# Kernel tuning notes

Hardware: AMD Instinct MI355X
Metric: run time of the kernel (lower is better)

Reference implementation:

```python
import jax, jax.numpy as jnp
import numpy as np

L, D, I, H, B, T, NBLK = 2, 2048, 5632, 16, 2, 1024, 4
EPS, TEMP, THETA = 1e-6, 1.0, 10000.0


def _rms_base(x):
    # RMSNorm without affine weight, computed in fp32 (matches _rms_norm_base)
    x = x.astype(jnp.float32)
    return x * jax.lax.rsqrt(jnp.mean(x * x, axis=-1, keepdims=True) + EPS)


def _rope(x):
    # x: [B,T,H,dh], rotate-half RoPE
    dh = x.shape[-1]
    inv = 1.0 / (THETA ** (jnp.arange(0, dh, 2, dtype=jnp.float32) / dh))
    t = jnp.arange(x.shape[1], dtype=jnp.float32)
    fr = jnp.outer(t, inv)  # [T, dh/2]
    cos = jnp.tile(jnp.cos(fr), (1, 2))[None, :, None, :]
    sin = jnp.tile(jnp.sin(fr), (1, 2))[None, :, None, :]
    x1, x2 = jnp.split(x, 2, axis=-1)
    return x * cos + jnp.concatenate([-x2, x1], axis=-1) * sin


def _attention(x, Wq, Wk, Wv, Wo):
    Bb, Tt, Dd = x.shape
    dh = Dd // H
    q = _rope((x @ Wq).reshape(Bb, Tt, H, dh))
    k = _rope((x @ Wk).reshape(Bb, Tt, H, dh))
    v = (x @ Wv).reshape(Bb, Tt, H, dh)
    s = jnp.einsum('bqhd,bkhd->bhqk', q, k) / jnp.sqrt(jnp.float32(dh))
    causal = jnp.tril(jnp.ones((Tt, Tt), bool))
    s = jnp.where(causal, s, jnp.float32(-1e30))
    a = jax.nn.softmax(s, axis=-1)
    return jnp.einsum('bhqk,bkhd->bqhd', a, v).reshape(Bb, Tt, Dd) @ Wo


def _forward(block_states, w_query_attn, key_norm_w_attn, w_query_mlp, key_norm_w_mlp,
             attn_norm_w, Wq, Wk, Wv, Wo, mlp_norm_w, Wgate, Wup, Wdown,
             active_mask, current_block_idx):
    n, Bb, Tt, Dd = block_states.shape
    scale = jnp.sqrt(jnp.float32(Dd)) * TEMP
    block_input = block_states[current_block_idx]
    mask = active_mask.astype(jnp.float32)[:, None, None]  # [B,1,1]

    # ---- phase 1: batch_attend_completed_blocks over all 2L routers ----
    # effective query = w_query * key_norm.weight (norm weight folded into query)
    q_eff = jnp.stack([w_query_attn * key_norm_w_attn,
                       w_query_mlp * key_norm_w_mlp], axis=1).reshape(2 * L, Dd)
    base_keys = _rms_base(block_states)                      # [n,B,T,D] fp32
    scores = jnp.einsum('qd,nbtd->qnbt', q_eff, base_keys) / scale
    mx = scores.max(axis=1)                                  # [q,B,T]
    ex = jnp.exp(scores - mx[:, None])                       # [q,n,B,T]
    lse = ex.sum(axis=1)                                     # [q,B,T]
    outs = jnp.einsum('qnbt,nbtd->qbtd', ex, block_states)   # unnormalized

    def merge(qi, partial):
        # merge_with_partial_block: online-softmax merge of phase1 stats with
        # the score of the current partial block
        if partial is None:
            return outs[qi] / lse[qi][..., None]
        ps = jnp.einsum('d,btd->bt', q_eff[qi], _rms_base(partial)) / scale
        m = jnp.maximum(mx[qi], ps)
        c1 = jnp.exp(mx[qi] - m)
        c2 = jnp.exp(ps - m)
        denom = c1 * lse[qi] + c2
        return (outs[qi] * (c1 * lse[qi] / denom)[..., None]
                + partial * (c2 / denom)[..., None])

    def blend(old, new):
        return new * mask + old * (1.0 - mask)

    def rmsn(x, w):
        return _rms_base(x) * w

    partial = None
    for i in range(L):
        attn_in = merge(2 * i, partial)
        attn_out = _attention(rmsn(attn_in, attn_norm_w[i]), Wq[i], Wk[i], Wv[i], Wo[i])
        old = block_input if partial is None else partial
        partial = blend(old, attn_out if partial is None else partial + attn_out)
        mlp_in = merge(2 * i + 1, partial)
        h = rmsn(mlp_in, mlp_norm_w[i])
        mlp_out = (jax.nn.silu(h @ Wgate[i]) * (h @ Wup[i])) @ Wdown[i]
        partial = blend(partial, partial + mlp_out)
    return partial


def setup_inputs() -> dict:
    key = jax.random.key(0)
    ks = jax.random.split(key, 12)
    p = lambda k, shape: jax.random.normal(k, shape, jnp.float32) * 0.02
    return {
        'block_states': jax.random.normal(ks[0], (NBLK, B, T, D), jnp.float32),
        'active_mask': jnp.ones((B,), bool),
        'w_query_attn': jax.random.normal(ks[1], (L, D), jnp.float32) * 0.02,
        'key_norm_w_attn': jnp.ones((L, D), jnp.float32),
        'w_query_mlp': jax.random.normal(ks[2], (L, D), jnp.float32) * 0.02,
        'key_norm_w_mlp': jnp.ones((L, D), jnp.float32),
        'attn_norm_w': jnp.ones((L, D), jnp.float32),
        'Wq': p(ks[3], (L, D, D)), 'Wk': p(ks[4], (L, D, D)),
        'Wv': p(ks[5], (L, D, D)), 'Wo': p(ks[6], (L, D, D)),
        'mlp_norm_w': jnp.ones((L, D), jnp.float32),
        'Wgate': p(ks[7], (L, D, I)), 'Wup': p(ks[8], (L, D, I)),
        'Wdown': p(ks[9], (L, I, D)),
        'current_block_idx': 3,
    }


def reference(block_states, active_mask, w_query_attn, key_norm_w_attn, w_query_mlp,
              key_norm_w_mlp, attn_norm_w, Wq, Wk, Wv, Wo, mlp_norm_w,
              Wgate, Wup, Wdown, current_block_idx):
    return _forward(block_states, w_query_attn, key_norm_w_attn, w_query_mlp,
                    key_norm_w_mlp, attn_norm_w, Wq, Wk, Wv, Wo, mlp_norm_w,
                    Wgate, Wup, Wdown, active_mask, current_block_idx)
```

## Files before the change

### kernel.cpp

```cpp
#include <hip/hip_runtime.h>

typedef unsigned short u16;
typedef __bf16 bf16x8 __attribute__((ext_vector_type(8)));
typedef float f32x4 __attribute__((ext_vector_type(4)));

__device__ __forceinline__ float u2f(unsigned int b){ union{unsigned int u; float f;} x; x.u=b; return x.f; }
__device__ __forceinline__ u16 f2b(float f){
  union{float fv; unsigned int u;} x; x.fv=f;
  unsigned int r = x.u + 0x7fffu + ((x.u>>16)&1u);
  return (u16)(r>>16);
}
__device__ __forceinline__ float b2f(u16 v){ return u2f(((unsigned int)v)<<16); }
__device__ __forceinline__ unsigned int pk2(float lo, float hi){
  return (unsigned int)f2b(lo) | ((unsigned int)f2b(hi)<<16);
}
__device__ __forceinline__ void load8(const float* p, float* o){
  float4 a = ((const float4*)p)[0], b = ((const float4*)p)[1];
  o[0]=a.x;o[1]=a.y;o[2]=a.z;o[3]=a.w;o[4]=b.x;o[5]=b.y;o[6]=b.z;o[7]=b.w;
}
__device__ __forceinline__ void gl_lds16(const u16* g, bf16x8* l){
  __builtin_amdgcn_global_load_lds((const __attribute__((address_space(1))) void*)g,
                                   (__attribute__((address_space(3))) void*)l, 16, 0, 0);
}

#define INV_SCALE 0.022097086912079608f
#define ATT_SCALE 0.08838834764831845f

__global__ __launch_bounds__(256) void mega0_kernel(
    const float* __restrict__ bs, const float* __restrict__ wqa, const float* __restrict__ kna,
    const float* __restrict__ wqm, const float* __restrict__ knm, const float* __restrict__ anw0,
    float* __restrict__ outs, float* __restrict__ mxb, float* __restrict__ lseb,
    u16* __restrict__ xnorm,
    const float* __restrict__ Wq, const float* __restrict__ Wk,
    const float* __restrict__ Wv, const float* __restrict__ Wo,
    const float* __restrict__ Wg, const float* __restrict__ Wu,
    const float* __restrict__ Wd,
    u16* __restrict__ WTall, u16* __restrict__ WTgu, u16* __restrict__ WTdd)
{
  int bb0 = blockIdx.x;
  if (bb0 < 2048){
    const int D=2048, M=2048;
    int m = bb0, t = threadIdx.x;
    int col = t*8;
    float x[4][8];
    #pragma unroll
    for (int n=0;n<4;n++) load8(bs + ((size_t)n*M + m)*D + col, x[n]);
    float qe[4][8];
    {
      float a[8], b[8];
      load8(wqa+col,a);   load8(kna+col,b);
      #pragma unroll
      for (int j=0;j<8;j++) qe[0][j]=a[j]*b[j];
      load8(wqm+col,a);   load8(knm+col,b);
      #pragma unroll
      for (int j=0;j<8;j++) qe[1][j]=a[j]*b[j];
      load8(wqa+D+col,a); load8(kna+D+col,b);
      #pragma unroll
      for (int j=0;j<8;j++) qe[2][j]=a[j]*b[j];
      load8(wqm+D+col,a); load8(knm+D+col,b);
      #pragma unroll
      for (int j=0;j<8;j++) qe[3][j]=a[j]*b[j];
    }
    float vals[20];
    #pragma unroll
    for (int n=0;n<4;n++){
      float s=0.f;
      #pragma unroll
      for (int j=0;j<8;j++) s += x[n][j]*x[n][j];
      vals[n]=s;
    }
    #pragma unroll
    for (int q=0;q<4;q++)
      #pragma unroll
      for (int n=0;n<4;n++){
        float s=0.f;
        #pragma unroll
        for (int j=0;j<8;j++) s += qe[q][j]*x[n][j];
        vals[4+q*4+n]=s;
      }
    #pragma unroll
    for (int s=0;s<20;s++){
      float v=vals[s];
      v+=__shfl_xor(v,1,64); v+=__shfl_xor(v,2,64); v+=__shfl_xor(v,4,64);
      v+=__shfl_xor(v,8,64); v+=__shfl_xor(v,16,64); v+=__shfl_xor(v,32,64);
      vals[s]=v;
    }
    __shared__ float red[20][4];
    __shared__ float redx[4];
    int w=t>>6, lane=t&63;
    if (lane==0){
      #pragma unroll
      for (int s=0;s<20;s++) red[s][w]=vals[s];
    }
    __syncthreads();
    float tot[20];
    #pragma unroll
    for (int s=0;s<20;s++) tot[s]=red[s][0]+red[s][1]+red[s][2]+red[s][3];
    float rn[4];
    #pragma unroll
    for (int n=0;n<4;n++) rn[n]=rsqrtf(tot[n]*(1.0f/2048.0f)+1e-6f);
    #pragma unroll
    for (int q=0;q<4;q++){
      float a0=tot[4+q*4+0]*rn[0]*INV_SCALE;
      float a1=tot[4+q*4+1]*rn[1]*INV_SCALE;
      float a2=tot[4+q*4+2]*rn[2]*INV_SCALE;
      float a3=tot[4+q*4+3]*rn[3]*INV_SCALE;
      float mx=fmaxf(fmaxf(a0,a1),fmaxf(a2,a3));
      float e0=__expf(a0-mx), e1=__expf(a1-mx), e2=__expf(a2-mx), e3=__expf(a3-mx);
      float lse=e0+e1+e2+e3;
      float ov[8];
      #pragma unroll
      for (int j=0;j<8;j++)
        ov[j]=e0*x[0][j]+e1*x[1][j]+e2*x[2][j]+e3*x[3][j];
      if (q==0){
        float inv = 1.0f/lse;
        float mg[8];
        #pragma unroll
        for (int j=0;j<8;j++) mg[j] = ov[j]*inv;
        float ssm=0.f;
        #pragma unroll
        for (int j=0;j<8;j++) ssm += mg[j]*mg[j];
        #pragma unroll
        for (int msk=1; msk<64; msk<<=1) ssm += __shfl_xor(ssm,msk,64);
        if (lane==0) redx[w]=ssm;
        __syncthreads();
        float st = redx[0]+redx[1]+redx[2]+redx[3];
        float r = rsqrtf(st*(1.0f/2048.0f)+1e-6f);
        float wv[8]; load8(anw0+col, wv);
        ushort4 o0, o1;
        o0.x=f2b(mg[0]*r*wv[0]); o0.y=f2b(mg[1]*r*wv[1]); o0.z=f2b(mg[2]*r*wv[2]); o0.w=f2b(mg[3]*r*wv[3]);
        o1.x=f2b(mg[4]*r*wv[4]); o1.y=f2b(mg[5]*r*wv[5]); o1.z=f2b(mg[6]*r*wv[6]); o1.w=f2b(mg[7]*r*wv[7]);
        size_t row = (size_t)m*D + col;
        ((ushort4*)(xnorm+row))[0]=o0; ((ushort4*)(xnorm+row))[1]=o1;
      } else {
        if (t==0){ mxb[(size_t)q*M+m]=mx; lseb[(size_t)q*M+m]=lse; }
        float* op = outs + ((size_t)q*M+m)*(size_t)D + col;
        float4 v0, v1;
        v0.x=ov[0]; v0.y=ov[1]; v0.z=ov[2]; v0.w=ov[3];
        v1.x=ov[4]; v1.y=ov[5]; v1.z=ov[6]; v1.w=ov[7];
        ((float4*)op)[0]=v0; ((float4*)op)[1]=v1;
      }
    }
    return;
  }
  int tid = threadIdx.x, wv = tid>>6, lane = tid&63;
  int tt = (bb0 - 2048)*4 + wv;
  const float* src; u16* dst; int K, N, kb, nb;
  if (tt < 8192){
    int z = tt >> 10, rem = tt & 1023;
    int x = rem & 31, y = rem >> 5;
    int wsel = z>>1, l = z&1;
    const float* s = (wsel==0)?Wq:(wsel==1)?Wk:(wsel==2)?Wv:Wo;
    src = s + (size_t)l*2048*2048;
    dst = WTall + (size_t)z*2048*2048;
    K=2048; N=2048; kb=y*64; nb=x*64;
  } else if (tt < 19456){
    int idx = tt - 8192;
    int z = idx / 2816, rem = idx % 2816;
    int x = rem % 88, y = rem / 88;
    int wsel = z>>1, l = z&1;
    const float* s = (wsel==0)?Wg:Wu;
    src = s + (size_t)l*2048*5632;
    dst = WTgu + (size_t)z*2048*5632;
    K=2048; N=5632; kb=y*64; nb=x*64;
  } else {
    int idx = tt - 19456;
    int l = idx / 2816, rem = idx % 2816;
    int x = rem % 32, y = rem / 32;
    src = Wd + (size_t)l*5632*2048;
    dst = WTdd + (size_t)l*5632*2048;
    K=5632; N=2048; kb=y*64; nb=x*64;
  }
  int kg = lane>>3, ng = lane&7;
  const float* sp = src + (size_t)(kb + kg*8)*N + nb + ng*8;
  float r[8][8];
  #pragma unroll
  for (int i=0;i<8;i++){
    float4 a = *(const float4*)(sp + (size_t)i*N);
    float4 b = *(const float4*)(sp + (size_t)i*N + 4);
    r[i][0]=a.x; r[i][1]=a.y; r[i][2]=a.z; r[i][3]=a.w;
    r[i][4]=b.x; r[i][5]=b.y; r[i][6]=b.z; r[i][7]=b.w;
  }
  u16* dp = dst + (size_t)(nb + ng*8)*K + kb + kg*8;
  #pragma unroll
  for (int j=0;j<8;j++){
    uint4 o;
    o.x = pk2(r[0][j], r[1][j]);
    o.y = pk2(r[2][j], r[3][j]);
    o.z = pk2(r[4][j], r[5][j]);
    o.w = pk2(r[6][j], r[7][j]);
    *(uint4*)(dp + (size_t)j*K) = o;
  }
}

__global__ __launch_bounds__(256) void ropevtrans_kernel(
    const u16* __restrict__ v, u16* __restrict__ vT,
    u16* __restrict__ qb, u16* __restrict__ kb)
{
  int bb = blockIdx.x;
  if (bb < 1024){
    __shared__ u16 tile[64][69];
    int x = bb & 15, y = (bb>>4) & 1, z = bb>>5;
    int b = z>>4, h = z&15;
    int t0 = x*64, d0 = y*64;
    int t = threadIdx.x;
    int c4 = (t&15)*4, r0 = t>>4;
    const u16* src = v + ((size_t)(b*1024) + t0)*2048 + h*128 + d0;
    #pragma unroll
    for (int p=0;p<4;p++){
      int tt = r0 + p*16;
      ushort4 val = *(const ushort4*)(src + (size_t)tt*2048 + c4);
      tile[tt][c4]=val.x; tile[tt][c4+1]=val.y; tile[tt][c4+2]=val.z; tile[tt][c4+3]=val.w;
    }
    __syncthreads();
    u16* dst = vT + ((size_t)z*128 + d0)*1024 + t0;
    #pragma unroll
    for (int p=0;p<4;p++){
      int dd = r0 + p*16;
      ushort4 o;
      o.x=tile[c4][dd]; o.y=tile[c4+1][dd]; o.z=tile[c4+2][dd]; o.w=tile[c4+3][dd];
      *(ushort4*)(dst + (size_t)dd*1024 + c4) = o;
    }
  } else {
    int idx = (bb-1024)*256 + threadIdx.x;
    int j  = idx & 63;
    int bt = idx >> 6;
    int t  = bt & 1023;
    float inv = __expf(-(float)j * (9.210340371976184f/64.0f));
    float fr = (float)t * inv;
    float cs, sn;
    sincosf(fr, &sn, &cs);
    size_t base0 = (size_t)bt*2048 + j;
    #pragma unroll
    for (int h=0; h<16; h++){
      size_t base = base0 + h*128;
      float x1 = b2f(qb[base]), x2 = b2f(qb[base+64]);
      qb[base]    = f2b(x1*cs - x2*sn);
      qb[base+64] = f2b(x2*cs + x1*sn);
      x1 = b2f(kb[base]); x2 = b2f(kb[base+64]);
      kb[base]    = f2b(x1*cs - x2*sn);
      kb[base+64] = f2b(x2*cs + x1*sn);
    }
  }
}

__global__ __launch_bounds__(256) void merge_norm_kernel(
    const float* __restrict__ outs_q, const float* __restrict__ mx_q, const float* __restrict__ lse_q,
    const float* __restrict__ partial, const float* __restrict__ wq, const float* __restrict__ kn,
    const float* __restrict__ nw, int has_partial, u16* __restrict__ xnorm)
{
  const int D=2048;
  int m = blockIdx.x, t = threadIdx.x, col = t*8;
  size_t row = (size_t)m*D + col;
  float o[8];
  load8(outs_q+row, o);
  float mx = mx_q[m], lse = lse_q[m];
  float mg[8];
  __shared__ float red[3][4];
  int w=t>>6, lane=t&63;
  if (has_partial){
    float p[8];
    load8(partial+row, p);
    float qv[8], kv[8];
    load8(wq+col,qv); load8(kn+col,kv);
    float ss=0.f, dp=0.f;
    #pragma unroll
    for (int j=0;j<8;j++){ ss += p[j]*p[j]; dp += qv[j]*kv[j]*p[j]; }
    #pragma unroll
    for (int msk=1; msk<64; msk<<=1){ ss += __shfl_xor(ss,msk,64); dp += __shfl_xor(dp,msk,64); }
    if (lane==0){ red[0][w]=ss; red[1][w]=dp; }
    __syncthreads();
    ss = red[0][0]+red[0][1]+red[0][2]+red[0][3];
    dp = red[1][0]+red[1][1]+red[1][2]+red[1][3];
    float ps = dp * rsqrtf(ss*(1.0f/2048.0f)+1e-6f) * INV_SCALE;
    float mm = fmaxf(mx, ps);
    float c1 = __expf(mx-mm), c2 = __expf(ps-mm);
    float denom = c1*lse + c2;
    float fo = c1*lse/denom, fp = c2/denom;
    #pragma unroll
    for (int j=0;j<8;j++) mg[j] = o[j]*fo + p[j]*fp;
  } else {
    float inv = 1.0f/lse;
    #pragma unroll
    for (int j=0;j<8;j++) mg[j] = o[j]*inv;
  }
  float ssm=0.f;
  #pragma unroll
  for (int j=0;j<8;j++) ssm += mg[j]*mg[j];
  #pragma unroll
  for (int msk=1; msk<64; msk<<=1) ssm += __shfl_xor(ssm,msk,64);
  if (lane==0) red[2][w]=ssm;
  __syncthreads();
  ssm = red[2][0]+red[2][1]+red[2][2]+red[2][3];
  float r = rsqrtf(ssm*(1.0f/2048.0f)+1e-6f);
  float wv[8]; load8(nw+col, wv);
  ushort4 o0, o1;
  o0.x=f2b(mg[0]*r*wv[0]); o0.y=f2b(mg[1]*r*wv[1]); o0.z=f2b(mg[2]*r*wv[2]); o0.w=f2b(mg[3]*r*wv[3]);
  o1.x=f2b(mg[4]*r*wv[4]); o1.y=f2b(mg[5]*r*wv[5]); o1.z=f2b(mg[6]*r*wv[6]); o1.w=f2b(mg[7]*r*wv[7]);
  ((ushort4*)(xnorm+row))[0]=o0; ((ushort4*)(xnorm+row))[1]=o1;
}

template<int BN, int OMODE>
__global__ __launch_bounds__(256) void gemm_tn(
    const u16* __restrict__ Abase, const u16* __restrict__ BTbase, size_t btz,
    u16* __restrict__ Cbb, size_t cbz, float* __restrict__ Cf, int beta, int N, int K, int KC)
{
  constexpr int WNT = BN/32;
  __shared__ bf16x8 As[1024];
  __shared__ bf16x8 Bs[BN*8];
  size_t koff = (OMODE==2) ? (size_t)blockIdx.z*KC : 0;
  const u16* A  = Abase  + (size_t)blockIdx.y*128*K + koff;
  const u16* BT = BTbase + (OMODE==2 ? (size_t)0 : btz*blockIdx.z) + (size_t)blockIdx.x*BN*K + koff;
  int tid = threadIdx.x;
  int wv = tid>>6, lane = tid&63, quad = lane>>4, l16 = lane&15;
  int wm = (wv&1)*64, wn = (wv>>1)*(BN/2);
  int wbase = tid & ~63;
  f32x4 acc[4][WNT];
  #pragma unroll
  for (int i=0;i<4;i++)
    #pragma unroll
    for (int j=0;j<WNT;j++){ f32x4 z={0.f,0.f,0.f,0.f}; acc[i][j]=z; }
  for (int kt=0; kt<KC; kt+=64){
    #pragma unroll
    for (int p=0;p<4;p++){
      int s = p*256+tid; int mm = s>>3; int kq = (s&7) ^ (mm&7);
      gl_lds16(A + (size_t)mm*K + kt + kq*8, &As[p*256 + wbase]);
    }
    #pragma unroll
    for (int p=0;p<BN/32;p++){
      int s = p*256+tid; int nn = s>>3; int kq = (s&7) ^ (nn&7);
      gl_lds16(BT + (size_t)nn*K + kt + kq*8, &Bs[p*256 + wbase]);
    }
    __syncthreads();
    #pragma unroll
    for (int kk=0;kk<2;kk++){
      int xq = (kk*4+quad) ^ (l16&7);
      bf16x8 af[4], bfr[WNT];
      #pragma unroll
      for (int mi=0;mi<4;mi++) af[mi] = As[(wm+mi*16+l16)*8 + xq];
      #pragma unroll
      for (int ni=0;ni<WNT;ni++) bfr[ni] = Bs[(wn+ni*16+l16)*8 + xq];
      #pragma unroll
      for (int mi=0;mi<4;mi++)
        #pragma unroll
        for (int ni=0;ni<WNT;ni++)
          acc[mi][ni] = __builtin_amdgcn_mfma_f32_16x16x32_bf16(af[mi], bfr[ni], acc[mi][ni], 0,0,0);
    }
    __syncthreads();
  }
  int row0 = blockIdx.y*128 + wm + quad*4;
  int col0 = blockIdx.x*BN + wn + l16;
  if (OMODE==1){
    #pragma unroll
    for (int mi=0;mi<4;mi++)
      #pragma unroll
      for (int ni=0;ni<WNT;ni++)
        #pragma unroll
        for (int r=0;r<4;r++){
          size_t idx = (size_t)(row0+mi*16+r)*N + (col0+ni*16);
          float pv = beta ? Cf[idx] : 0.0f;
          Cf[idx] = pv + acc[mi][ni][r];
        }
  } else if (OMODE==2){
    #pragma unroll
    for (int mi=0;mi<4;mi++)
      #pragma unroll
      for (int ni=0;ni<WNT;ni++)
        #pragma unroll
        for (int r=0;r<4;r++){
          size_t idx = (size_t)(row0+mi*16+r)*N + (col0+ni*16);
          unsafeAtomicAdd(&Cf[idx], acc[mi][ni][r]);
        }
  } else {
    u16* Cb = Cbb + cbz*blockIdx.z;
    #pragma unroll
    for (int mi=0;mi<4;mi++)
      #pragma unroll
      for (int ni=0;ni<WNT;ni++)
        #pragma unroll
        for (int r=0;r<4;r++){
          size_t idx = (size_t)(row0+mi*16+r)*N + (col0+ni*16);
          Cb[idx] = f2b(acc[mi][ni][r]);
        }
  }
}

__global__ __launch_bounds__(256,2) void gemm_gateup(
    const u16* __restrict__ Abase, const u16* __restrict__ Gb, const u16* __restrict__ Ub,
    u16* __restrict__ HG, int N, int K)
{
  __shared__ bf16x8 As[1024];
  __shared__ bf16x8 Gs[1024];
  __shared__ bf16x8 Us[1024];
  const u16* A = Abase + (size_t)blockIdx.y*128*K;
  const u16* G = Gb + (size_t)blockIdx.x*128*K;
  const u16* U = Ub + (size_t)blockIdx.x*128*K;
  int tid = threadIdx.x;
  int wv = tid>>6, lane = tid&63, quad = lane>>4, l16 = lane&15;
  int wm = (wv&1)*64, wn = (wv>>1)*64;
  int wbase = tid & ~63;
  f32x4 ag[4][4], au[4][4];
  #pragma unroll
  for (int i=0;i<4;i++)
    #pragma unroll
    for (int j=0;j<4;j++){ f32x4 z={0.f,0.f,0.f,0.f}; ag[i][j]=z; au[i][j]=z; }
  for (int kt=0; kt<K; kt+=64){
    #pragma unroll
    for (int p=0;p<4;p++){
      int s = p*256+tid; int mm = s>>3; int kq = (s&7) ^ (mm&7);
      size_t off = (size_t)mm*K + kt + kq*8;
      gl_lds16(A + off, &As[p*256 + wbase]);
      gl_lds16(G + off, &Gs[p*256 + wbase]);
      gl_lds16(U + off, &Us[p*256 + wbase]);
    }
    __syncthreads();
    #pragma unroll
    for (int kk=0;kk<2;kk++){
      int xq = (kk*4+quad) ^ (l16&7);
      bf16x8 af[4], gf[4], uf[4];
      #pragma unroll
      for (int mi=0;mi<4;mi++) af[mi] = As[(wm+mi*16+l16)*8 + xq];
      #pragma unroll
      for (int ni=0;ni<4;ni++){ gf[ni] = Gs[(wn+ni*16+l16)*8 + xq]; uf[ni] = Us[(wn+ni*16+l16)*8 + xq]; }
      #pragma unroll
      for (int mi=0;mi<4;mi++)
        #pragma unroll
        for (int ni=0;ni<4;ni++){
          ag[mi][ni] = __builtin_amdgcn_mfma_f32_16x16x32_bf16(af[mi], gf[ni], ag[mi][ni], 0,0,0);
          au[mi][ni] = __builtin_amdgcn_mfma_f32_16x16x32_bf16(af[mi], uf[ni], au[mi][ni], 0,0,0);
        }
    }
    __syncthreads();
  }
  int row0 = blockIdx.y*128 + wm + quad*4;
  int col0 = blockIdx.x*128 + wn + l16;
  #pragma unroll
  for (int mi=0;mi<4;mi++)
    #pragma unroll
    for (int ni=0;ni<4;ni++)
      #pragma unroll
      for (int r=0;r<4;r++){
        float g = ag[mi][ni][r], u = au[mi][ni][r];
        float h = g/(1.0f+__expf(-g))*u;
        HG[(size_t)(row0+mi*16+r)*N + (col0+ni*16)] = f2b(h);
      }
}

__global__ __launch_bounds__(256,3) void attn_kernel(
    const u16* __restrict__ q, const u16* __restrict__ k, const u16* __restrict__ vT,
    u16* __restrict__ o)
{
  const int T=1024, D=2048;
  int qt = (int)gridDim.x - 1 - (int)blockIdx.x;
  int b = blockIdx.y>>4;
  int h = blockIdx.y & 15;
  __shared__ bf16x8 Ks[2][1024];
  __shared__ bf16x8 Vs[1024];
  __shared__ bf16x8 Ps[4][4][16];
  int tid=threadIdx.x, w=tid>>6, lane=tid&63, quad=lane>>4, l16=lane&15;
  int wbase = tid & ~63;

  const u16* qp = q + ((size_t)(b*T + qt*64 + w*16 + l16))*D + h*128 + quad*8;
  bf16x8 qreg[4];
  #pragma unroll
  for (int kk=0;kk<4;kk++) qreg[kk] = *(const bf16x8*)(qp + kk*32);

  const u16* kb0 = k + ((size_t)(b*T))*D + h*128;
  const u16* vtp = vT + (size_t)blockIdx.y*128*1024;

  auto stageK = [&](int kt, int buf){
    #pragma unroll
    for (int p=0;p<4;p++){
      int s=p*256+tid; int kr=s>>4; int kq=(s&15) ^ (kr&15);
      gl_lds16(kb0 + (size_t)(kt*64+kr)*D + kq*8, &Ks[buf][p*256 + wbase]);
    }
  };
  auto stageV = [&](int kt){
    #pragma unroll
    for (int p=0;p<4;p++){
      int s=p*256+tid; int d=s>>3; int kq=(s&7) ^ (d&7);
      gl_lds16(vtp + (size_t)d*1024 + kt*64 + kq*8, &Vs[p*256 + wbase]);
    }
  };

  f32x4 oacc[8];
  #pragma unroll
  for (int i=0;i<8;i++){ f32x4 z={0.f,0.f,0.f,0.f}; oacc[i]=z; }
  float mi[4], li[4];
  #pragma unroll
  for (int r=0;r<4;r++){ mi[r]=-INFINITY; li[r]=0.f; }

  stageK(0, 0);
  stageV(0);
  __syncthreads();

  int cur = 0;
  for (int kt=0; kt<=qt; kt++){
    if (kt < qt) stageK(kt+1, cur^1);
    f32x4 s[4];
    #pragma unroll
    for (int ni=0;ni<4;ni++){ f32x4 z={0.f,0.f,0.f,0.f}; s[ni]=z; }
    __builtin_amdgcn_s_setprio(1);
    #pragma unroll
    for (int kk=0;kk<4;kk++){
      int xq = (kk*4+quad) ^ l16;
      #pragma unroll
      for (int ni=0;ni<4;ni++)
        s[ni] = __builtin_amdgcn_mfma_f32_16x16x32_bf16(qreg[kk], Ks[cur][(ni*16+l16)*16 + xq], s[ni], 0,0,0);
    }
    __builtin_amdgcn_s_setprio(0);
    int qrow = qt*64 + w*16 + quad*4;
    #pragma unroll
    for (int ni=0;ni<4;ni++)
      #pragma unroll
      for (int r=0;r<4;r++){
        float val = s[ni][r]*ATT_SCALE;
        int kc = kt*64 + ni*16 + l16;
        if (kc > qrow + r) val = -1e30f;
        s[ni][r] = val;
      }
    float rmax[4];
    #pragma unroll
    for (int r=0;r<4;r++) rmax[r] = fmaxf(fmaxf(s[0][r],s[1][r]), fmaxf(s[2][r],s[3][r]));
    #pragma unroll
    for (int r=0;r<4;r++){
      rmax[r]=fmaxf(rmax[r],__shfl_xor(rmax[r],1,64));
      rmax[r]=fmaxf(rmax[r],__shfl_xor(rmax[r],2,64));
      rmax[r]=fmaxf(rmax[r],__shfl_xor(rmax[r],4,64));
      rmax[r]=fmaxf(rmax[r],__shfl_xor(rmax[r],8,64));
    }
    float mnew[4], alpha[4], rsum[4];
    #pragma unroll
    for (int r=0;r<4;r++) mnew[r]=fmaxf(mi[r],rmax[r]);
    #pragma unroll
    for (int ni=0;ni<4;ni++)
      #pragma unroll
      for (int r=0;r<4;r++) s[ni][r]=__expf(s[ni][r]-mnew[r]);
    #pragma unroll
    for (int r=0;r<4;r++){
      rsum[r]=s[0][r]+s[1][r]+s[2][r]+s[3][r];
      rsum[r]+=__shfl_xor(rsum[r],1,64);
      rsum[r]+=__shfl_xor(rsum[r],2,64);
      rsum[r]+=__shfl_xor(rsum[r],4,64);
      rsum[r]+=__shfl_xor(rsum[r],8,64);
      alpha[r]=__expf(mi[r]-mnew[r]);
      li[r]=li[r]*alpha[r]+rsum[r];
      mi[r]=mnew[r];
    }
    #pragma unroll
    for (int dn=0;dn<8;dn++){
      oacc[dn][0]*=alpha[0]; oacc[dn][1]*=alpha[1];
      oacc[dn][2]*=alpha[2]; oacc[dn][3]*=alpha[3];
    }
    __syncthreads();
    u16* Pp = (u16*)&Ps[w][0][0];
    #pragma unroll
    for (int h2=0;h2<2;h2++){
      #pragma unroll
      for (int nj=0;nj<2;nj++){
        int ni = h2*2 + nj;
        #pragma unroll
        for (int r=0;r<4;r++){
          int kc = ni*16+l16;
          Pp[((((kc>>3)&3)*16) + quad*4 + r)*8 + (kc&7)] = f2b(s[ni][r]);
        }
      }
      int xv = (h2*4+quad) ^ (l16&7);
      __builtin_amdgcn_s_setprio(1);
      bf16x8 pa = Ps[w][quad][l16];
      #pragma unroll
      for (int dn=0;dn<8;dn++)
        oacc[dn] = __builtin_amdgcn_mfma_f32_16x16x32_bf16(pa, Vs[(dn*16+l16)*8 + xv], oacc[dn], 0,0,0);
      __builtin_amdgcn_s_setprio(0);
    }
    __syncthreads();
    if (kt < qt) stageV(kt+1);
    cur ^= 1;
  }
  size_t obase = ((size_t)(b*T + qt*64 + w*16 + quad*4))*D + h*128 + l16;
  #pragma unroll
  for (int dn=0;dn<8;dn++)
    #pragma unroll
    for (int r=0;r<4;r++)
      o[obase + (size_t)r*D + dn*16] = f2b(oacc[dn][r]/li[r]);
}

extern "C" void kernel_launch(void* const* d_in, const int* in_sizes, int n_in,
                              void* d_out, int out_size, void* d_ws, size_t ws_size,
                              hipStream_t stream) {
  (void)in_sizes; (void)n_in; (void)out_size; (void)ws_size;
  const size_t D=2048, I=5632, M=2048;
  const size_t MD=M*D, MI=M*I, LDD=2*D*D, LDI=2*D*I;

  const float* bs  = (const float*)d_in[0];
  const float* wqa = (const float*)d_in[2];
  const float* kna = (const float*)d_in[3];
  const float* wqm = (const float*)d_in[4];
  const float* knm = (const float*)d_in[5];
  const float* anw = (const float*)d_in[6];
  const float* Wq  = (const float*)d_in[7];
  const float* Wk  = (const float*)d_in[8];
  const float* Wv  = (const float*)d_in[9];
  const float* Wo  = (const float*)d_in[10];
  const float* mnw = (const float*)d_in[11];
  const float* Wg  = (const float*)d_in[12];
  const float* Wu  = (const float*)d_in[13];
  const float* Wd  = (const float*)d_in[14];

  char* wsp = (char*)d_ws;
  auto alloc = [&](size_t bytes){ char* p = wsp; wsp += (bytes + 255) & ~(size_t)255; return p; };
  u16*   WTall  = (u16*)  alloc(4*LDD*2);
  u16*   WTgu   = (u16*)  alloc(2*LDI*2);
  u16*   WTd    = (u16*)  alloc(LDI*2);
  float* outs   = (float*)alloc(4*MD*4);
  float* mxb    = (float*)alloc(4*M*4);
  float* lseb   = (float*)alloc(4*M*4);
  u16*   xnorm  = (u16*)  alloc(MD*2);
  u16*   qkv    = (u16*)  alloc(3*MD*2);
  u16*   vt     = (u16*)  alloc(MD*2);
  u16*   attno  = (u16*)  alloc(MD*2);
  u16*   hg     = (u16*)  alloc(MI*2);
  float* partial = (float*)d_out;

  mega0_kernel<<<8320,256,0,stream>>>(bs, wqa, kna, wqm, knm, anw, outs, mxb, lseb, xnorm,
                                      Wq, Wk, Wv, Wo, Wg, Wu, Wd, WTall, WTgu, WTd);

  u16* WTo = WTall + 3*LDD;
  for (int i=0;i<2;i++){
    if (i>0)
      merge_norm_kernel<<<2048,256,0,stream>>>(outs + (size_t)(2*i)*MD, mxb + (size_t)(2*i)*M,
          lseb + (size_t)(2*i)*M, partial, wqa + i*D, kna + i*D, anw + i*D, 1, xnorm);
    gemm_tn<128,0><<<dim3(16,16,3),256,0,stream>>>(xnorm, WTall + (size_t)i*D*D, LDD,
        qkv, MD, nullptr, 0, 2048, 2048, 2048);
    ropevtrans_kernel<<<1536,256,0,stream>>>(qkv+2*MD, vt, qkv, qkv+MD);
    attn_kernel<<<dim3(16,32),256,0,stream>>>(qkv, qkv+MD, vt, attno);
    if (i==0)
      gemm_tn<64,1><<<dim3(32,16,1),256,0,stream>>>(attno, WTo, 0,
          nullptr, 0, partial, 0, 2048, 2048, 2048);
    else
      gemm_tn<128,2><<<dim3(16,16,2),256,0,stream>>>(attno, WTo + (size_t)i*D*D, 0,
          nullptr, 0, partial, 1, 2048, 2048, 1024);
    merge_norm_kernel<<<2048,256,0,stream>>>(outs + (size_t)(2*i+1)*MD, mxb + (size_t)(2*i+1)*M,
        lseb + (size_t)(2*i+1)*M, partial, wqm + i*D, knm + i*D, mnw + i*D, 1, xnorm);
    gemm_gateup<<<dim3(44,16),256,0,stream>>>(xnorm, WTgu + (size_t)i*I*D, WTgu + LDI + (size_t)i*I*D,
        hg, 5632, 2048);
    gemm_tn<128,2><<<dim3(16,16,2),256,0,stream>>>(hg, WTd + (size_t)i*D*I, 0,
        nullptr, 0, partial, 1, 2048, 5632, 2816);
  }
}
```

Baseline: 1.185 ms.

## Overlap remaining weight transposes with the first-layer QKV GEMM

Result: no change. 1.192 ms (+0.6%).

```diff
diff --git a/kernel.cpp b/kernel.cpp
--- a/kernel.cpp
+++ b/kernel.cpp
@@ -26,125 +26,11 @@
 #define INV_SCALE 0.022097086912079608f
 #define ATT_SCALE 0.08838834764831845f
 
-__global__ __launch_bounds__(256) void mega0_kernel(
-    const float* __restrict__ bs, const float* __restrict__ wqa, const float* __restrict__ kna,
-    const float* __restrict__ wqm, const float* __restrict__ knm, const float* __restrict__ anw0,
-    float* __restrict__ outs, float* __restrict__ mxb, float* __restrict__ lseb,
-    u16* __restrict__ xnorm,
-    const float* __restrict__ Wq, const float* __restrict__ Wk,
-    const float* __restrict__ Wv, const float* __restrict__ Wo,
-    const float* __restrict__ Wg, const float* __restrict__ Wu,
-    const float* __restrict__ Wd,
-    u16* __restrict__ WTall, u16* __restrict__ WTgu, u16* __restrict__ WTdd)
+__device__ __forceinline__ void rtrans_tile(int tt, int lane,
+    const float* Wq, const float* Wk, const float* Wv, const float* Wo,
+    const float* Wg, const float* Wu, const float* Wd,
+    u16* WTall, u16* WTgu, u16* WTdd)
 {
-  int bb0 = blockIdx.x;
-  if (bb0 < 2048){
-    const int D=2048, M=2048;
-    int m = bb0, t = threadIdx.x;
-    int col = t*8;
-    float x[4][8];
-    #pragma unroll
-    for (int n=0;n<4;n++) load8(bs + ((size_t)n*M + m)*D + col, x[n]);
-    float qe[4][8];
-    {
-      float a[8], b[8];
-      load8(wqa+col,a);   load8(kna+col,b);
-      #pragma unroll
-      for (int j=0;j<8;j++) qe[0][j]=a[j]*b[j];
-      load8(wqm+col,a);   load8(knm+col,b);
-      #pragma unroll
-      for (int j=0;j<8;j++) qe[1][j]=a[j]*b[j];
-      load8(wqa+D+col,a); load8(kna+D+col,b);
-      #pragma unroll
-      for (int j=0;j<8;j++) qe[2][j]=a[j]*b[j];
-      load8(wqm+D+col,a); load8(knm+D+col,b);
-      #pragma unroll
-      for (int j=0;j<8;j++) qe[3][j]=a[j]*b[j];
-    }
-    float vals[20];
-    #pragma unroll
-    for (int n=0;n<4;n++){
-      float s=0.f;
-      #pragma unroll
-      for (int j=0;j<8;j++) s += x[n][j]*x[n][j];
-      vals[n]=s;
-    }
-    #pragma unroll
-    for (int q=0;q<4;q++)
-      #pragma unroll
-      for (int n=0;n<4;n++){
-        float s=0.f;
-        #pragma unroll
-        for (int j=0;j<8;j++) s += qe[q][j]*x[n][j];
-        vals[4+q*4+n]=s;
-      }
-    #pragma unroll
-    for (int s=0;s<20;s++){
-      float v=vals[s];
-      v+=__shfl_xor(v,1,64); v+=__shfl_xor(v,2,64); v+=__shfl_xor(v,4,64);
-      v+=__shfl_xor(v,8,64); v+=__shfl_xor(v,16,64); v+=__shfl_xor(v,32,64);
-      vals[s]=v;
-    }
-    __shared__ float red[20][4];
-    __shared__ float redx[4];
-    int w=t>>6, lane=t&63;
-    if (lane==0){
-      #pragma unroll
-      for (int s=0;s<20;s++) red[s][w]=vals[s];
-    }
-    __syncthreads();
-    float tot[20];
-    #pragma unroll
-    for (int s=0;s<20;s++) tot[s]=red[s][0]+red[s][1]+red[s][2]+red[s][3];
-    float rn[4];
-    #pragma unroll
-    for (int n=0;n<4;n++) rn[n]=rsqrtf(tot[n]*(1.0f/2048.0f)+1e-6f);
-    #pragma unroll
-    for (int q=0;q<4;q++){
-      float a0=tot[4+q*4+0]*rn[0]*INV_SCALE;
-      float a1=tot[4+q*4+1]*rn[1]*INV_SCALE;
-      float a2=tot[4+q*4+2]*rn[2]*INV_SCALE;
-      float a3=tot[4+q*4+3]*rn[3]*INV_SCALE;
-      float mx=fmaxf(fmaxf(a0,a1),fmaxf(a2,a3));
-      float e0=__expf(a0-mx), e1=__expf(a1-mx), e2=__expf(a2-mx), e3=__expf(a3-mx);
-      float lse=e0+e1+e2+e3;
-      float ov[8];
-      #pragma unroll
-      for (int j=0;j<8;j++)
-        ov[j]=e0*x[0][j]+e1*x[1][j]+e2*x[2][j]+e3*x[3][j];
-      if (q==0){
-        float inv = 1.0f/lse;
-        float mg[8];
-        #pragma unroll
-        for (int j=0;j<8;j++) mg[j] = ov[j]*inv;
-        float ssm=0.f;
-        #pragma unroll
-        for (int j=0;j<8;j++) ssm += mg[j]*mg[j];
-        #pragma unroll
-        for (int msk=1; msk<64; msk<<=1) ssm += __shfl_xor(ssm,msk,64);
-        if (lane==0) redx[w]=ssm;
-        __syncthreads();
-        float st = redx[0]+redx[1]+redx[2]+redx[3];
-        float r = rsqrtf(st*(1.0f/2048.0f)+1e-6f);
-        float wv[8]; load8(anw0+col, wv);
-        ushort4 o0, o1;
-        o0.x=f2b(mg[0]*r*wv[0]); o0.y=f2b(mg[1]*r*wv[1]); o0.z=f2b(mg[2]*r*wv[2]); o0.w=f2b(mg[3]*r*wv[3]);
-        o1.x=f2b(mg[4]*r*wv[4]); o1.y=f2b(mg[5]*r*wv[5]); o1.z=f2b(mg[6]*r*wv[6]); o1.w=f2b(mg[7]*r*wv[7]);
-        size_t row = (size_t)m*D + col;
-        ((ushort4*)(xnorm+row))[0]=o0; ((ushort4*)(xnorm+row))[1]=o1;
-      } else {
-        if (t==0){ mxb[(size_t)q*M+m]=mx; lseb[(size_t)q*M+m]=lse; }
-        float* op = outs + ((size_t)q*M+m)*(size_t)D + col;
-        float4 v0, v1;
-        v0.x=ov[0]; v0.y=ov[1]; v0.z=ov[2]; v0.w=ov[3];
-        v1.x=ov[4]; v1.y=ov[5]; v1.z=ov[6]; v1.w=ov[7];
-        ((float4*)op)[0]=v0; ((float4*)op)[1]=v1;
-      }
-    }
-    return;
-  }
-  int tid = threadIdx.x, wv = tid>>6, lane = tid&63;
-  int tt = (bb0 - 2048)*4 + wv;
   const float* src; u16* dst; int K, N, kb, nb;
   if (tt < 8192){
     int z = tt >> 10, rem = tt & 1023;
@@ -193,6 +79,200 @@
   }
 }
 
+__global__ __launch_bounds__(256) void mega0_kernel(
+    const float* __restrict__ bs, const float* __restrict__ wqa, const float* __restrict__ kna,
+    const float* __restrict__ wqm, const float* __restrict__ knm, const float* __restrict__ anw0,
+    float* __restrict__ outs, float* __restrict__ mxb, float* __restrict__ lseb,
+    u16* __restrict__ xnorm,
+    const float* __restrict__ Wq, const float* __restrict__ Wk,
+    const float* __restrict__ Wv, const float* __restrict__ Wo,
+    const float* __restrict__ Wg, const float* __restrict__ Wu,
+    const float* __restrict__ Wd,
+    u16* __restrict__ WTall, u16* __restrict__ WTgu, u16* __restrict__ WTdd)
+{
+  int bb0 = blockIdx.x;
+  if (bb0 < 2048){
+    const int D=2048, M=2048;
+    int m = bb0, t = threadIdx.x;
+    int col = t*8;
+    float x[4][8];
+    #pragma unroll
+    for (int n=0;n<4;n++) load8(bs + ((size_t)n*M + m)*D + col, x[n]);
+    float qe[4][8];
+    {
+      float a[8], b[8];
+      load8(wqa+col,a);   load8(kna+col,b);
+      #pragma unroll
+      for (int j=0;j<8;j++) qe[0][j]=a[j]*b[j];
+      load8(wqm+col,a);   load8(knm+col,b);
+      #pragma unroll
+      for (int j=0;j<8;j++) qe[1][j]=a[j]*b[j];
+      load8(wqa+D+col,a); load8(kna+D+col,b);
+      #pragma unroll
+      for (int j=0;j<8;j++) qe[2][j]=a[j]*b[j];
+      load8(wqm+D+col,a); load8(knm+D+col,b);
+      #pragma unroll
+      for (int j=0;j<8;j++) qe[3][j]=a[j]*b[j];
+    }
+    float vals[20];
+    #pragma unroll
+    for (int n=0;n<4;n++){
+      float s=0.f;
+      #pragma unroll
+      for (int j=0;j<8;j++) s += x[n][j]*x[n][j];
+      vals[n]=s;
+    }
+    #pragma unroll
+    for (int q=0;q<4;q++)
+      #pragma unroll
+      for (int n=0;n<4;n++){
+        float s=0.f;
+        #pragma unroll
+        for (int j=0;j<8;j++) s += qe[q][j]*x[n][j];
+        vals[4+q*4+n]=s;
+      }
+    #pragma unroll
+    for (int s=0;s<20;s++){
+      float v=vals[s];
+      v+=__shfl_xor(v,1,64); v+=__shfl_xor(v,2,64); v+=__shfl_xor(v,4,64);
+      v+=__shfl_xor(v,8,64); v+=__shfl_xor(v,16,64); v+=__shfl_xor(v,32,64);
+      vals[s]=v;
+    }
+    __shared__ float red[20][4];
+    __shared__ float redx[4];
+    int w=t>>6, lane=t&63;
+    if (lane==0){
+      #pragma unroll
+      for (int s=0;s<20;s++) red[s][w]=vals[s];
+    }
+    __syncthreads();
+    float tot[20];
+    #pragma unroll
+    for (int s=0;s<20;s++) tot[s]=red[s][0]+red[s][1]+red[s][2]+red[s][3];
+    float rn[4];
+    #pragma unroll
+    for (int n=0;n<4;n++) rn[n]=rsqrtf(tot[n]*(1.0f/2048.0f)+1e-6f);
+    #pragma unroll
+    for (int q=0;q<4;q++){
+      float a0=tot[4+q*4+0]*rn[0]*INV_SCALE;
+      float a1=tot[4+q*4+1]*rn[1]*INV_SCALE;
+      float a2=tot[4+q*4+2]*rn[2]*INV_SCALE;
+      float a3=tot[4+q*4+3]*rn[3]*INV_SCALE;
+      float mx=fmaxf(fmaxf(a0,a1),fmaxf(a2,a3));
+      float e0=__expf(a0-mx), e1=__expf(a1-mx), e2=__expf(a2-mx), e3=__expf(a3-mx);
+      float lse=e0+e1+e2+e3;
+      float ov[8];
+      #pragma unroll
+      for (int j=0;j<8;j++)
+        ov[j]=e0*x[0][j]+e1*x[1][j]+e2*x[2][j]+e3*x[3][j];
+      if (q==0){
+        float inv = 1.0f/lse;
+        float mg[8];
+        #pragma unroll
+        for (int j=0;j<8;j++) mg[j] = ov[j]*inv;
+        float ssm=0.f;
+        #pragma unroll
+        for (int j=0;j<8;j++) ssm += mg[j]*mg[j];
+        #pragma unroll
+        for (int msk=1; msk<64; msk<<=1) ssm += __shfl_xor(ssm,msk,64);
+        if (lane==0) redx[w]=ssm;
+        __syncthreads();
+        float st = redx[0]+redx[1]+redx[2]+redx[3];
+        float r = rsqrtf(st*(1.0f/2048.0f)+1e-6f);
+        float wv[8]; load8(anw0+col, wv);
+        ushort4 o0, o1;
+        o0.x=f2b(mg[0]*r*wv[0]); o0.y=f2b(mg[1]*r*wv[1]); o0.z=f2b(mg[2]*r*wv[2]); o0.w=f2b(mg[3]*r*wv[3]);
+        o1.x=f2b(mg[4]*r*wv[4]); o1.y=f2b(mg[5]*r*wv[5]); o1.z=f2b(mg[6]*r*wv[6]); o1.w=f2b(mg[7]*r*wv[7]);
+        size_t row = (size_t)m*D + col;
+        ((ushort4*)(xnorm+row))[0]=o0; ((ushort4*)(xnorm+row))[1]=o1;
+      } else {
+        if (t==0){ mxb[(size_t)q*M+m]=mx; lseb[(size_t)q*M+m]=lse; }
+        float* op = outs + ((size_t)q*M+m)*(size_t)D + col;
+        float4 v0, v1;
+        v0.x=ov[0]; v0.y=ov[1]; v0.z=ov[2]; v0.w=ov[3];
+        v1.x=ov[4]; v1.y=ov[5]; v1.z=ov[6]; v1.w=ov[7];
+        ((float4*)op)[0]=v0; ((float4*)op)[1]=v1;
+      }
+    }
+    return;
+  }
+  int tid = threadIdx.x, wv = tid>>6, lane = tid&63;
+  int tt = (bb0 - 2048)*4 + wv;
+  rtrans_tile(tt, lane, Wq, Wk, Wv, Wo, Wg, Wu, Wd, WTall, WTgu, WTdd);
+}
+
+__global__ __launch_bounds__(256) void qkvt_kernel(
+    const u16* __restrict__ Abase, const u16* __restrict__ BTbase, size_t btz,
+    u16* __restrict__ Cbb, size_t cbz, int N, int K,
+    const float* __restrict__ Wq, const float* __restrict__ Wk,
+    const float* __restrict__ Wv, const float* __restrict__ Wo,
+    const float* __restrict__ Wg, const float* __restrict__ Wu,
+    const float* __restrict__ Wd,
+    u16* __restrict__ WTall, u16* __restrict__ WTgu, u16* __restrict__ WTdd)
+{
+  int bb0 = blockIdx.x;
+  if (bb0 < 768){
+    __shared__ bf16x8 As[1024];
+    __shared__ bf16x8 Bs[1024];
+    int bx = bb0 & 15, by = (bb0>>4)&15, bz = bb0>>8;
+    const u16* A  = Abase  + (size_t)by*128*K;
+    const u16* BT = BTbase + btz*bz + (size_t)bx*128*K;
+    int tid = threadIdx.x;
+    int wv = tid>>6, lane = tid&63, quad = lane>>4, l16 = lane&15;
+    int wm = (wv&1)*64, wn = (wv>>1)*64;
+    int wbase = tid & ~63;
+    f32x4 acc[4][4];
+    #pragma unroll
+    for (int i=0;i<4;i++)
+      #pragma unroll
+      for (int j=0;j<4;j++){ f32x4 z={0.f,0.f,0.f,0.f}; acc[i][j]=z; }
+    for (int kt=0; kt<K; kt+=64){
+      #pragma unroll
+      for (int p=0;p<4;p++){
+        int s = p*256+tid; int mm = s>>3; int kq = (s&7) ^ (mm&7);
+        gl_lds16(A + (size_t)mm*K + kt + kq*8, &As[p*256 + wbase]);
+      }
+      #pragma unroll
+      for (int p=0;p<4;p++){
+        int s = p*256+tid; int nn = s>>3; int kq = (s&7) ^ (nn&7);
+        gl_lds16(BT + (size_t)nn*K + kt + kq*8, &Bs[p*256 + wbase]);
+      }
+      __syncthreads();
+      #pragma unroll
+      for (int kk=0;kk<2;kk++){
+        int xq = (kk*4+quad) ^ (l16&7);
+        bf16x8 af[4], bfr[4];
+        #pragma unroll
+        for (int mi=0;mi<4;mi++) af[mi] = As[(wm+mi*16+l16)*8 + xq];
+        #pragma unroll
+        for (int ni=0;ni<4;ni++) bfr[ni] = Bs[(wn+ni*16+l16)*8 + xq];
+        #pragma unroll
+        for (int mi=0;mi<4;mi++)
+          #pragma unroll
+          for (int ni=0;ni<4;ni++)
+            acc[mi][ni] = __builtin_amdgcn_mfma_f32_16x16x32_bf16(af[mi], bfr[ni], acc[mi][ni], 0,0,0);
+      }
+      __syncthreads();
+    }
+    int row0 = by*128 + wm + quad*4;
+    int col0 = bx*128 + wn + l16;
+    u16* Cb = Cbb + cbz*bz;
+    #pragma unroll
+    for (int mi=0;mi<4;mi++)
+      #pragma unroll
+      for (int ni=0;ni<4;ni++)
+        #pragma unroll
+        for (int r=0;r<4;r++){
+          size_t idx = (size_t)(row0+mi*16+r)*N + (col0+ni*16);
+          Cb[idx] = f2b(acc[mi][ni][r]);
+        }
+    return;
+  }
+  int tid = threadIdx.x, wv = tid>>6, lane = tid&63;
+  int tt = (bb0 - 768)*4 + wv + 6144;
+  rtrans_tile(tt, lane, Wq, Wk, Wv, Wo, Wg, Wu, Wd, WTall, WTgu, WTdd);
+}
+
 __global__ __launch_bounds__(256) void ropevtrans_kernel(
     const u16* __restrict__ v, u16* __restrict__ vT,
     u16* __restrict__ qb, u16* __restrict__ kb)
@@ -622,7 +702,7 @@
   u16*   hg     = (u16*)  alloc(MI*2);
   float* partial = (float*)d_out;
 
-  mega0_kernel<<<8320,256,0,stream>>>(bs, wqa, kna, wqm, knm, anw, outs, mxb, lseb, xnorm,
+  mega0_kernel<<<3584,256,0,stream>>>(bs, wqa, kna, wqm, knm, anw, outs, mxb, lseb, xnorm,
                                       Wq, Wk, Wv, Wo, Wg, Wu, Wd, WTall, WTgu, WTd);
 
   u16* WTo = WTall + 3*LDD;
@@ -630,8 +710,12 @@
     if (i>0)
       merge_norm_kernel<<<2048,256,0,stream>>>(outs + (size_t)(2*i)*MD, mxb + (size_t)(2*i)*M,
           lseb + (size_t)(2*i)*M, partial, wqa + i*D, kna + i*D, anw + i*D, 1, xnorm);
-    gemm_tn<128,0><<<dim3(16,16,3),256,0,stream>>>(xnorm, WTall + (size_t)i*D*D, LDD,
-        qkv, MD, nullptr, 0, 2048, 2048, 2048);
+    if (i==0)
+      qkvt_kernel<<<5504,256,0,stream>>>(xnorm, WTall, LDD, qkv, MD, 2048, 2048,
+          Wq, Wk, Wv, Wo, Wg, Wu, Wd, WTall, WTgu, WTd);
+    else
+      gemm_tn<128,0><<<dim3(16,16,3),256,0,stream>>>(xnorm, WTall + (size_t)i*D*D, LDD,
+          qkv, MD, nullptr, 0, 2048, 2048, 2048);
     ropevtrans_kernel<<<1536,256,0,stream>>>(qkv+2*MD, vt, qkv, qkv+MD);
     attn_kernel<<<dim3(16,32),256,0,stream>>>(qkv, qkv+MD, vt, attno);
     if (i==0)
```
